# Kernel optimization log

Hardware: AMD Instinct MI355X
Metric: run time of the kernel (lower is better)

Reference implementation:

```python
import jax, jax.numpy as jnp
import numpy as np

B, T, E, H, L = 32, 2048, 256, 256, 2


def setup_inputs() -> dict:
    key = jax.random.key(0)
    k = jax.random.split(key, 6)
    x = jax.random.normal(k[0], (B, T, E), jnp.float32)
    h0 = jax.random.normal(k[1], (L, B, H), jnp.float32)
    # weights scaled to avoid tanh saturation (mimics fan-in init)
    W0 = jax.random.normal(k[2], (E + H, H), jnp.float32) * 0.05
    b0 = jax.random.normal(k[3], (H,), jnp.float32) * 0.05
    W1 = jax.random.normal(k[4], (2 * H, H), jnp.float32) * 0.05
    b1 = jax.random.normal(k[5], (H,), jnp.float32) * 0.05
    return {"x": x, "h0": h0, "W0": W0, "b0": b0, "W1": W1, "b1": b1}


def reference(x, h0, W0, b0, W1, b1):
    # x: [B,T,E]; h0: [L,B,H] (torch permutes to [B,L,H])
    h_init = jnp.transpose(h0, (1, 0, 2))  # [B,L,H]
    Ws = (W0, W1)
    bs = (b0, b1)

    def step(h, x_t):  # h: [B,L,H], x_t: [B,E]
        inp = x_t
        new_h = []
        for l in range(L):  # small fixed stack of cells
            z = jnp.concatenate([inp, h[:, l, :]], axis=-1) @ Ws[l] + bs[l]
            ht = jnp.tanh(z)  # [B,H]
            inp = ht
            new_h.append(ht)
        return jnp.stack(new_h, axis=1), ht  # carry, per-step top-layer output

    x_tbe = jnp.transpose(x, (1, 0, 2))  # [T,B,E]
    h_final, outs = jax.lax.scan(step, h_init, x_tbe)
    hidden_states = jnp.transpose(outs, (1, 0, 2))  # [B,T,H]
    ht = h_final[:, -1:, :]  # final top-layer state, [B,1,H]
    return hidden_states, ht
```

## Files before the change

### kernel.cpp

```cpp
#include <hip/hip_runtime.h>


typedef _Float16 half2_t __attribute__((ext_vector_type(2)));

#define TT 2048
#define BB 32
#define XPB 8
#define CHUNK 64
#define NCHUNK (TT / CHUNK)

__device__ __forceinline__ unsigned packw(float lo, float hi) {
    half2_t r;
    r.x = (_Float16)lo;
    r.y = (_Float16)hi;
    return __builtin_bit_cast(unsigned, r);
}
#define H2(X) __builtin_bit_cast(half2_t, (X))

#define LDS_BARRIER() asm volatile("s_waitcnt lgkmcnt(0)\n\ts_barrier" ::: "memory")

__device__ __forceinline__ int rload(int* pf) {
    return __hip_atomic_load(pf, __ATOMIC_RELAXED, __HIP_MEMORY_SCOPE_AGENT);
}
__device__ __forceinline__ void astore(int* pf, int v) {
    __hip_atomic_store(pf, v, __ATOMIC_RELEASE, __HIP_MEMORY_SCOPE_AGENT);
}
#define ACQUIRE_FENCE() __builtin_amdgcn_fence(__ATOMIC_ACQUIRE, "agent")

#define KAW8(B)                                                             \
    "+v"(wp[(B)]), "+v"(wp[(B) + 1]), "+v"(wp[(B) + 2]), "+v"(wp[(B) + 3]), \
    "+v"(wp[(B) + 4]), "+v"(wp[(B) + 5]), "+v"(wp[(B) + 6]), "+v"(wp[(B) + 7])
#define KEEPALIVE()                                                  \
    asm volatile("" : KAW8(0), KAW8(8), KAW8(16), KAW8(24));         \
    asm volatile("" : KAW8(32), KAW8(40), KAW8(48), KAW8(56));       \
    asm volatile("" : KAW8(64), KAW8(72), KAW8(80), KAW8(88));       \
    asm volatile("" : KAW8(96), KAW8(104), KAW8(112), KAW8(120));

#define FDOT(H, W_, A) A = __builtin_amdgcn_fdot2(H2(H), H2(W_), A, false)
#define FD4(H, K)               \
    FDOT(H, wp[(K)], ac0);      \
    FDOT(H, wp[32 + (K)], ac1); \
    FDOT(H, wp[64 + (K)], ac2); \
    FDOT(H, wp[96 + (K)], ac3);

#define DOTS()                                                          \
    float ac0 = 0.f, ac1 = 0.f, ac2 = 0.f, ac3 = 0.f;                   \
    {                                                                   \
        const uint4* hp_ = hbq + 9 * p;                                 \
        uint4 q0 = hp_[0], q1 = hp_[1], q2 = hp_[2], q3 = hp_[3];       \
        uint4 q4 = hp_[4], q5 = hp_[5], q6 = hp_[6], q7 = hp_[7];       \
        FD4(q0.x, 0)  FD4(q0.y, 1)  FD4(q0.z, 2)  FD4(q0.w, 3)         \
        FD4(q1.x, 4)  FD4(q1.y, 5)  FD4(q1.z, 6)  FD4(q1.w, 7)         \
        FD4(q2.x, 8)  FD4(q2.y, 9)  FD4(q2.z, 10) FD4(q2.w, 11)        \
        FD4(q3.x, 12) FD4(q3.y, 13) FD4(q3.z, 14) FD4(q3.w, 15)        \
        FD4(q4.x, 16) FD4(q4.y, 17) FD4(q4.z, 18) FD4(q4.w, 19)        \
        FD4(q5.x, 20) FD4(q5.y, 21) FD4(q5.z, 22) FD4(q5.w, 23)        \
        FD4(q6.x, 24) FD4(q6.y, 25) FD4(q6.z, 26) FD4(q6.w, 27)        \
        FD4(q7.x, 28) FD4(q7.y, 29) FD4(q7.z, 30) FD4(q7.w, 31)        \
    }

#define BFLY(x)                                                              \
    asm("v_add_f32_dpp %0, %0, %0 quad_perm:[1,0,3,2] row_mask:0xf "         \
        "bank_mask:0xf"                                                      \
        : "+v"(x));                                                          \
    asm("v_add_f32_dpp %0, %0, %0 quad_perm:[2,3,0,1] row_mask:0xf "         \
        "bank_mask:0xf"                                                      \
        : "+v"(x));

#define LOAD_WP4(Wm, rowbase, p_, jg_)                                       \
    _Pragma("unroll")                                                        \
    for (int c = 0; c < 4; ++c) {                                            \
        _Pragma("unroll")                                                    \
        for (int k = 0; k < 32; ++k) {                                       \
            const int col_ = (jg_) + 64 * c;                                 \
            wp[c * 32 + k] =                                                 \
                packw((Wm)[(size_t)((rowbase) + 64 * (p_) + 2 * k) * 256 +   \
                           col_],                                            \
                      (Wm)[(size_t)((rowbase) + 64 * (p_) + 2 * k + 1) * 256 \
                           + col_]);                                         \
        }                                                                    \
    }

__device__ __forceinline__ int sidx_of(int i) {
    return 72 * (i >> 6) + (i & 63);
}

template <bool ALIAS>
__device__ __forceinline__ void proj_rows(
    const float* __restrict__ src, float* __restrict__ dst,
    unsigned (&wp)[128], float bj, int nrows, uint4 (*hb)[36], int tid,
    int p, int jg, int col)
{
    _Float16* st0 = reinterpret_cast<_Float16*>(hb[0]);
    _Float16* st1 = reinterpret_cast<_Float16*>(hb[1]);
    const int si = sidx_of(tid);
    st0[si] = (_Float16)src[tid];
    __syncthreads();
    for (int r = 0; r < nrows; ++r) {
        KEEPALIVE()
        _Float16* stn = (r & 1) ? st0 : st1;
        if (r + 1 < nrows) stn[si] = (_Float16)src[(size_t)(r + 1) * 256 + tid];
        const uint4* hbq = hb[r & 1];
        DOTS()
        BFLY(ac0) BFLY(ac1) BFLY(ac2) BFLY(ac3)
        float z = (p == 0) ? ac0 : ((p == 1) ? ac1 : ((p == 2) ? ac2 : ac3));
        dst[(size_t)r * 256 + col] = z + bj;
        if (ALIAS) __syncthreads();
        else LDS_BARRIER();
    }
}

template <bool WAIT, bool PUB>
__device__ __forceinline__ void scan_core(
    const float* __restrict__ W, const float* __restrict__ h_init,
    const float* __restrict__ xsrc, float* __restrict__ hdst, float* hfinal,
    int* pubflag, int* waitflags, uint4 (*hb)[36], int tid)
{
    const int p = tid & 3;
    const int jg = tid >> 2;
    const int col = jg + 64 * p;

    unsigned wp[128];
    LOAD_WP4(W, 256, p, jg)

    _Float16* hw0 = reinterpret_cast<_Float16*>(hb[0]);
    _Float16* hw1 = reinterpret_cast<_Float16*>(hb[1]);
    hw0[sidx_of(tid)] = (_Float16)h_init[tid];
    const int wsi = 72 * p + jg;

    float xpc[XPB], xpn[XPB], hs[XPB];

    auto step = [&](int t, float xp) -> float {
        KEEPALIVE()
        const uint4* hbq = hb[t & 1];
        DOTS()
        BFLY(ac0) BFLY(ac1) BFLY(ac2) BFLY(ac3)
        float z = (p == 0) ? ac0 : ((p == 1) ? ac1 : ((p == 2) ? ac2 : ac3));
        z += xp;
        const float e = __expf(2.0f * z);
        const float hn = 1.0f - 2.0f / (e + 1.0f);
        _Float16* dstw = ((t + 1) & 1) ? hw1 : hw0;
        dstw[wsi] = (_Float16)hn;
        LDS_BARRIER();
        return hn;
    };

    __syncthreads();
    for (int chunk = 0; chunk < NCHUNK; ++chunk) {
        const int tbase = chunk * CHUNK;
        if (WAIT) {
            while (rload(&waitflags[chunk]) == 0) __builtin_amdgcn_s_sleep(1);
            ACQUIRE_FENCE();
        }
#pragma unroll
        for (int u = 0; u < XPB; ++u)
            xpc[u] = xsrc[(size_t)(tbase + u) * 256 + col];
        for (int g = 0; g < CHUNK / XPB; ++g) {
            const int t0 = tbase + g * XPB;
            if (g + 1 < CHUNK / XPB) {
#pragma unroll
                for (int u = 0; u < XPB; ++u)
                    xpn[u] = xsrc[(size_t)(t0 + XPB + u) * 256 + col];
            }
#pragma unroll
            for (int u = 0; u < XPB; ++u) hs[u] = step(t0 + u, xpc[u]);
#pragma unroll
            for (int u = 0; u < XPB; ++u)
                hdst[(size_t)(t0 + u) * 256 + col] = hs[u];
            if (t0 + XPB == TT && hfinal != nullptr) hfinal[col] = hs[XPB - 1];
            if (g + 1 < CHUNK / XPB) {
#pragma unroll
                for (int u = 0; u < XPB; ++u) xpc[u] = xpn[u];
            }
        }
        if (PUB) {
            __syncthreads();
            if (tid == 0) astore(pubflag, tbase + CHUNK);
        }
    }
}

template <bool ALIAS>
__global__ __launch_bounds__(256, 1) void proj23_kernel(
    const float* in, const float* __restrict__ W, const float* __restrict__ bias,
    float* out, int rows_per_wg)
{
    __shared__ uint4 hb[2][36];
    const int tid = threadIdx.x;
    const int p = tid & 3;
    const int jg = tid >> 2;
    const int col = jg + 64 * p;
    unsigned wp[128];
    LOAD_WP4(W, 0, p, jg)
    const float bj = bias[col];
    const size_t r0 = (size_t)blockIdx.x * rows_per_wg;
    proj_rows<ALIAS>(in + r0 * 256, out + r0 * 256, wp, bj, rows_per_wg, hb,
                     tid, p, jg, col);
}

__global__ __launch_bounds__(256, 1) void scan23_kernel(
    const float* __restrict__ W, const float* __restrict__ h_init,
    float* __restrict__ io, float* __restrict__ hfinal)
{
    __shared__ uint4 hb[2][36];
    const int b = blockIdx.x;
    scan_core<false, false>(W, h_init + b * 256, io + (size_t)b * TT * 256,
                            io + (size_t)b * TT * 256,
                            hfinal ? hfinal + b * 256 : nullptr, nullptr,
                            nullptr, hb, threadIdx.x);
}

__global__ __launch_bounds__(256, 1) void mega23_kernel(
    const float* __restrict__ x, const float* __restrict__ W0,
    const float* __restrict__ b0v, const float* __restrict__ W1,
    const float* __restrict__ b1v, const float* __restrict__ h0init,
    float* xpA, float* out, int* flags)
{
    __shared__ uint4 hb[2][36];
    const int tid = threadIdx.x;
    const int bid = blockIdx.x;
    int* flagL0 = flags;
    int* chunkdone = flags + BB * 16;
    int* xp0done = flags + BB * 16 + BB * NCHUNK;

    if (bid < BB) {
        const int b = bid;
        scan_core<true, true>(W0, h0init + b * 256, xpA + (size_t)b * TT * 256,
                              out + (size_t)b * TT * 256, nullptr,
                              &flagL0[b * 16], &xp0done[b * NCHUNK], hb, tid);
    } else if (bid < 3 * BB) {
        const int k = bid - BB;
        const int b = k >> 1;
        const int half = k & 1;
        const int p = tid & 3;
        const int jg = tid >> 2;
        const int col = jg + 64 * p;

        unsigned wp[128];
        LOAD_WP4(W1, 0, p, jg)
        const float bj = b1v[col];

        for (int chunk = half; chunk < NCHUNK; chunk += 2) {
            while (rload(&flagL0[b * 16]) < (chunk + 1) * CHUNK)
                __builtin_amdgcn_s_sleep(1);
            ACQUIRE_FENCE();
            const int tbase = chunk * CHUNK;
            const float* src = out + ((size_t)b * TT + tbase) * 256;
            float* dst = xpA + ((size_t)b * TT + tbase) * 256;
            proj_rows<false>(src, dst, wp, bj, CHUNK, hb, tid, p, jg, col);
            __syncthreads();
            if (tid == 0) astore(&chunkdone[b * NCHUNK + chunk], 1);
        }
    } else if (bid < 4 * BB) {
        const int b = bid - 3 * BB;
        scan_core<true, false>(W1, h0init + (size_t)(BB + b) * 256,
                               xpA + (size_t)b * TT * 256,
                               out + (size_t)b * TT * 256,
                               out + (size_t)BB * TT * 256 + b * 256, nullptr,
                               &chunkdone[b * NCHUNK], hb, tid);
    } else {
        const int k = bid - 4 * BB;
        const int b = k >> 1;
        const int half = k & 1;
        const int p = tid & 3;
        const int jg = tid >> 2;
        const int col = jg + 64 * p;

        unsigned wp[128];
        LOAD_WP4(W0, 0, p, jg)
        const float bj = b0v[col];

        for (int chunk = half; chunk < NCHUNK; chunk += 2) {
            const int tbase = chunk * CHUNK;
            const float* src = x + ((size_t)b * TT + tbase) * 256;
            float* dst = xpA + ((size_t)b * TT + tbase) * 256;
            proj_rows<false>(src, dst, wp, bj, CHUNK, hb, tid, p, jg, col);
            __syncthreads();
            if (tid == 0) astore(&xp0done[b * NCHUNK + chunk], 1);
        }
    }
}

extern "C" void kernel_launch(void* const* d_in, const int* in_sizes, int n_in,
                              void* d_out, int out_size, void* d_ws, size_t ws_size,
                              hipStream_t stream) {
    const float* x  = (const float*)d_in[0];
    const float* h0 = (const float*)d_in[1];
    const float* W0 = (const float*)d_in[2];
    const float* b0 = (const float*)d_in[3];
    const float* W1 = (const float*)d_in[4];
    const float* b1 = (const float*)d_in[5];
    float* out = (float*)d_out;

    const size_t XPA_FLOATS = (size_t)BB * TT * 256;
    const size_t FLAG_INTS = (size_t)BB * 16 + 2 * (size_t)BB * NCHUNK;
    const size_t NEEDED = XPA_FLOATS * 4 + FLAG_INTS * 4;

    if (ws_size >= NEEDED) {
        float* xpA = (float*)d_ws;
        int* flags = (int*)((char*)d_ws + XPA_FLOATS * 4);
        hipMemsetAsync(flags, 0, FLAG_INTS * 4, stream);
        mega23_kernel<<<6 * BB, 256, 0, stream>>>(x, W0, b0, W1, b1, h0, xpA,
                                                  out, flags);
    } else {
        proj23_kernel<true><<<512, 256, 0, stream>>>(x, W0, b0, out, 128);
        scan23_kernel<<<BB, 256, 0, stream>>>(W0, h0, out, nullptr);
        proj23_kernel<true><<<512, 256, 0, stream>>>(out, W1, b1, out, 128);
        scan23_kernel<<<BB, 256, 0, stream>>>(W1, h0 + BB * 256, out,
                                              out + XPA_FLOATS);
    }
}
```

Baseline: 1.188 ms.

## Fuse layer-0 scan, layer-1 projection and layer-1 scan into one wavefront-pipelined workgroup

Replaces the multi-block mega kernel with two launches. A chaser kernel computes the layer-0 input projection into a workspace and sets per-chunk flags. A fused kernel then runs one 768-thread workgroup per batch element, where three 256-thread groups skew layer-0 recurrence, layer-1 input projection and layer-1 recurrence by one step each and exchange data through LDS ring buffers. This removes the global-memory round trip and cross-workgroup flag polling between layers, but every step now pays a 768-thread barrier and register pressure rises at the larger block size. XPB is also reduced from 8 to 4.

```diff
diff --git a/kernel.cpp b/kernel.cpp
--- a/kernel.cpp
+++ b/kernel.cpp
@@ -5,7 +5,7 @@
 
 #define TT 2048
 #define BB 32
-#define XPB 8
+#define XPB 4
 #define CHUNK 64
 #define NCHUNK (TT / CHUNK)
 
@@ -110,78 +110,179 @@
     }
 }
 
-template <bool WAIT, bool PUB>
-__device__ __forceinline__ void scan_core(
+__device__ __forceinline__ void scan_serial(
     const float* __restrict__ W, const float* __restrict__ h_init,
     const float* __restrict__ xsrc, float* __restrict__ hdst, float* hfinal,
-    int* pubflag, int* waitflags, uint4 (*hb)[36], int tid)
+    uint4 (*hb)[36], int tid)
 {
     const int p = tid & 3;
     const int jg = tid >> 2;
     const int col = jg + 64 * p;
-
     unsigned wp[128];
     LOAD_WP4(W, 256, p, jg)
-
     _Float16* hw0 = reinterpret_cast<_Float16*>(hb[0]);
     _Float16* hw1 = reinterpret_cast<_Float16*>(hb[1]);
     hw0[sidx_of(tid)] = (_Float16)h_init[tid];
     const int wsi = 72 * p + jg;
-
-    float xpc[XPB], xpn[XPB], hs[XPB];
-
-    auto step = [&](int t, float xp) -> float {
+    __syncthreads();
+    float hn = 0.f;
+    for (int t = 0; t < TT; ++t) {
         KEEPALIVE()
         const uint4* hbq = hb[t & 1];
         DOTS()
         BFLY(ac0) BFLY(ac1) BFLY(ac2) BFLY(ac3)
         float z = (p == 0) ? ac0 : ((p == 1) ? ac1 : ((p == 2) ? ac2 : ac3));
-        z += xp;
+        z += xsrc[(size_t)t * 256 + col];
         const float e = __expf(2.0f * z);
-        const float hn = 1.0f - 2.0f / (e + 1.0f);
+        hn = 1.0f - 2.0f / (e + 1.0f);
         _Float16* dstw = ((t + 1) & 1) ? hw1 : hw0;
         dstw[wsi] = (_Float16)hn;
+        hdst[(size_t)t * 256 + col] = hn;
         LDS_BARRIER();
-        return hn;
+    }
+    if (hfinal != nullptr) hfinal[col] = hn;
+}
+
+__global__ __launch_bounds__(256, 1) void chaser0_kernel(
+    const float* __restrict__ x, const float* __restrict__ W0,
+    const float* __restrict__ b0v, float* xpA, int* xp0done)
+{
+    __shared__ uint4 hb[2][36];
+    const int tid = threadIdx.x;
+    const int k = blockIdx.x;
+    const int b = k >> 2;
+    const int quarter = k & 3;
+    const int p = tid & 3;
+    const int jg = tid >> 2;
+    const int col = jg + 64 * p;
+
+    unsigned wp[128];
+    LOAD_WP4(W0, 0, p, jg)
+    const float bj = b0v[col];
+
+    for (int chunk = quarter; chunk < NCHUNK; chunk += 4) {
+        const int tbase = chunk * CHUNK;
+        const float* src = x + ((size_t)b * TT + tbase) * 256;
+        float* dst = xpA + ((size_t)b * TT + tbase) * 256;
+        proj_rows<false>(src, dst, wp, bj, CHUNK, hb, tid, p, jg, col);
+        __syncthreads();
+        if (tid == 0) astore(&xp0done[b * NCHUNK + chunk], 1);
+    }
+}
+
+__global__ __launch_bounds__(768, 3) void fused24_kernel(
+    const float* __restrict__ xpA, const float* __restrict__ W0,
+    const float* __restrict__ W1, const float* __restrict__ b1v,
+    const float* __restrict__ h0init, float* __restrict__ out, int* xp0done)
+{
+    __shared__ __align__(16) _Float16 h0ring[3][288];
+    __shared__ float xp1ring[2][264];
+    __shared__ __align__(16) _Float16 h1buf[2][288];
+
+    const int tid = threadIdx.x;
+    const int grp = tid >> 8;
+    const int ltid = tid & 255;
+    const int p = ltid & 3;
+    const int jg = ltid >> 2;
+    const int col = jg + 64 * p;
+    const int b = blockIdx.x;
+
+    unsigned wp[128];
+    if (grp == 0) {
+        LOAD_WP4(W0, 256, p, jg)
+    } else if (grp == 1) {
+        LOAD_WP4(W1, 0, p, jg)
+    } else {
+        LOAD_WP4(W1, 256, p, jg)
+    }
+    const float bj = (grp == 1) ? b1v[col] : 0.f;
+
+    if (grp == 0) h0ring[2][sidx_of(ltid)] = (_Float16)h0init[b * 256 + ltid];
+    if (grp == 2)
+        h1buf[0][sidx_of(ltid)] = (_Float16)h0init[(size_t)(BB + b) * 256 + ltid];
+
+    const float* xsrc = xpA + (size_t)b * TT * 256;
+    float* hdst = out + (size_t)b * TT * 256;
+    int* myflags = xp0done + b * NCHUNK;
+    __syncthreads();
+
+    float xpc[XPB], xpn[XPB];
+
+    auto STEP = [&](int s, float xp0) {
+        KEEPALIVE()
+        if (grp == 0) {
+            if (s < TT) {
+                const uint4* hbq = (const uint4*)h0ring[(s + 2) % 3];
+                DOTS()
+                BFLY(ac0) BFLY(ac1) BFLY(ac2) BFLY(ac3)
+                float z = (p == 0) ? ac0
+                        : (p == 1) ? ac1 : ((p == 2) ? ac2 : ac3);
+                z += xp0;
+                const float e = __expf(2.0f * z);
+                const float hn = 1.0f - 2.0f / (e + 1.0f);
+                h0ring[s % 3][72 * p + jg] = (_Float16)hn;
+            }
+        } else if (grp == 1) {
+            if (s >= 1 && s <= TT) {
+                const int t = s - 1;
+                const uint4* hbq = (const uint4*)h0ring[t % 3];
+                DOTS()
+                BFLY(ac0) BFLY(ac1) BFLY(ac2) BFLY(ac3)
+                float z = (p == 0) ? ac0
+                        : (p == 1) ? ac1 : ((p == 2) ? ac2 : ac3);
+                xp1ring[t & 1][66 * p + jg] = z + bj;
+            }
+        } else {
+            if (s >= 2) {
+                const int t = s - 2;
+                const float xp = xp1ring[t & 1][66 * p + jg];
+                const uint4* hbq = (const uint4*)h1buf[t & 1];
+                DOTS()
+                BFLY(ac0) BFLY(ac1) BFLY(ac2) BFLY(ac3)
+                float z = (p == 0) ? ac0
+                        : (p == 1) ? ac1 : ((p == 2) ? ac2 : ac3);
+                z += xp;
+                const float e = __expf(2.0f * z);
+                const float hn = 1.0f - 2.0f / (e + 1.0f);
+                h1buf[(t + 1) & 1][72 * p + jg] = (_Float16)hn;
+                hdst[(size_t)t * 256 + col] = hn;
+                if (t == TT - 1)
+                    out[(size_t)BB * TT * 256 + b * 256 + col] = hn;
+            }
+        }
+        LDS_BARRIER();
     };
 
-    __syncthreads();
     for (int chunk = 0; chunk < NCHUNK; ++chunk) {
         const int tbase = chunk * CHUNK;
-        if (WAIT) {
-            while (rload(&waitflags[chunk]) == 0) __builtin_amdgcn_s_sleep(1);
+        if (grp == 0) {
+            while (rload(&myflags[chunk]) == 0) __builtin_amdgcn_s_sleep(1);
             ACQUIRE_FENCE();
+#pragma unroll
+            for (int u = 0; u < XPB; ++u)
+                xpc[u] = xsrc[(size_t)(tbase + u) * 256 + col];
         }
-#pragma unroll
-        for (int u = 0; u < XPB; ++u)
-            xpc[u] = xsrc[(size_t)(tbase + u) * 256 + col];
         for (int g = 0; g < CHUNK / XPB; ++g) {
-            const int t0 = tbase + g * XPB;
-            if (g + 1 < CHUNK / XPB) {
+            const int s0 = tbase + g * XPB;
+            if (grp == 0 && g + 1 < CHUNK / XPB) {
 #pragma unroll
                 for (int u = 0; u < XPB; ++u)
-                    xpn[u] = xsrc[(size_t)(t0 + XPB + u) * 256 + col];
+                    xpn[u] = xsrc[(size_t)(s0 + XPB + u) * 256 + col];
             }
 #pragma unroll
-            for (int u = 0; u < XPB; ++u) hs[u] = step(t0 + u, xpc[u]);
-#pragma unroll
-            for (int u = 0; u < XPB; ++u)
-                hdst[(size_t)(t0 + u) * 256 + col] = hs[u];
-            if (t0 + XPB == TT && hfinal != nullptr) hfinal[col] = hs[XPB - 1];
-            if (g + 1 < CHUNK / XPB) {
+            for (int u = 0; u < XPB; ++u) STEP(s0 + u, xpc[u]);
+            if (grp == 0 && g + 1 < CHUNK / XPB) {
 #pragma unroll
                 for (int u = 0; u < XPB; ++u) xpc[u] = xpn[u];
             }
         }
-        if (PUB) {
-            __syncthreads();
-            if (tid == 0) astore(pubflag, tbase + CHUNK);
-        }
-    }
+    }
+    STEP(TT, 0.f);
+    STEP(TT + 1, 0.f);
 }
 
 template <bool ALIAS>
-__global__ __launch_bounds__(256, 1) void proj23_kernel(
+__global__ __launch_bounds__(256, 1) void proj24_kernel(
     const float* in, const float* __restrict__ W, const float* __restrict__ bias,
     float* out, int rows_per_wg)
 {
@@ -198,87 +299,15 @@
                      tid, p, jg, col);
 }
 
-__global__ __launch_bounds__(256, 1) void scan23_kernel(
+__global__ __launch_bounds__(256, 1) void scan24_kernel(
     const float* __restrict__ W, const float* __restrict__ h_init,
     float* __restrict__ io, float* __restrict__ hfinal)
 {
     __shared__ uint4 hb[2][36];
     const int b = blockIdx.x;
-    scan_core<false, false>(W, h_init + b * 256, io + (size_t)b * TT * 256,
-                            io + (size_t)b * TT * 256,
-                            hfinal ? hfinal + b * 256 : nullptr, nullptr,
-                            nullptr, hb, threadIdx.x);
-}
-
-__global__ __launch_bounds__(256, 1) void mega23_kernel(
-    const float* __restrict__ x, const float* __restrict__ W0,
-    const float* __restrict__ b0v, const float* __restrict__ W1,
-    const float* __restrict__ b1v, const float* __restrict__ h0init,
-    float* xpA, float* out, int* flags)
-{
-    __shared__ uint4 hb[2][36];
-    const int tid = threadIdx.x;
-    const int bid = blockIdx.x;
-    int* flagL0 = flags;
-    int* chunkdone = flags + BB * 16;
-    int* xp0done = flags + BB * 16 + BB * NCHUNK;
-
-    if (bid < BB) {
-        const int b = bid;
-        scan_core<true, true>(W0, h0init + b * 256, xpA + (size_t)b * TT * 256,
-                              out + (size_t)b * TT * 256, nullptr,
-                              &flagL0[b * 16], &xp0done[b * NCHUNK], hb, tid);
-    } else if (bid < 3 * BB) {
-        const int k = bid - BB;
-        const int b = k >> 1;
-        const int half = k & 1;
-        const int p = tid & 3;
-        const int jg = tid >> 2;
-        const int col = jg + 64 * p;
-
-        unsigned wp[128];
-        LOAD_WP4(W1, 0, p, jg)
-        const float bj = b1v[col];
-
-        for (int chunk = half; chunk < NCHUNK; chunk += 2) {
-            while (rload(&flagL0[b * 16]) < (chunk + 1) * CHUNK)
-                __builtin_amdgcn_s_sleep(1);
-            ACQUIRE_FENCE();
-            const int tbase = chunk * CHUNK;
-            const float* src = out + ((size_t)b * TT + tbase) * 256;
-            float* dst = xpA + ((size_t)b * TT + tbase) * 256;
-            proj_rows<false>(src, dst, wp, bj, CHUNK, hb, tid, p, jg, col);
-            __syncthreads();
-            if (tid == 0) astore(&chunkdone[b * NCHUNK + chunk], 1);
-        }
-    } else if (bid < 4 * BB) {
-        const int b = bid - 3 * BB;
-        scan_core<true, false>(W1, h0init + (size_t)(BB + b) * 256,
-                               xpA + (size_t)b * TT * 256,
-                               out + (size_t)b * TT * 256,
-                               out + (size_t)BB * TT * 256 + b * 256, nullptr,
-                               &chunkdone[b * NCHUNK], hb, tid);
-    } else {
-        const int k = bid - 4 * BB;
-        const int b = k >> 1;
-        const int half = k & 1;
-        const int p = tid & 3;
-        const int jg = tid >> 2;
-        const int col = jg + 64 * p;
-
-        unsigned wp[128];
-        LOAD_WP4(W0, 0, p, jg)
-        const float bj = b0v[col];
-
-        for (int chunk = half; chunk < NCHUNK; chunk += 2) {
-            const int tbase = chunk * CHUNK;
-            const float* src = x + ((size_t)b * TT + tbase) * 256;
-            float* dst = xpA + ((size_t)b * TT + tbase) * 256;
-            proj_rows<false>(src, dst, wp, bj, CHUNK, hb, tid, p, jg, col);
-            __syncthreads();
-            if (tid == 0) astore(&xp0done[b * NCHUNK + chunk], 1);
-        }
-    }
+    scan_serial(W, h_init + b * 256, io + (size_t)b * TT * 256,
+                io + (size_t)b * TT * 256,
+                hfinal ? hfinal + b * 256 : nullptr, hb, threadIdx.x);
 }
 
 extern "C" void kernel_launch(void* const* d_in, const int* in_sizes, int n_in,
@@ -293,20 +322,20 @@
     float* out = (float*)d_out;
 
     const size_t XPA_FLOATS = (size_t)BB * TT * 256;
-    const size_t FLAG_INTS = (size_t)BB * 16 + 2 * (size_t)BB * NCHUNK;
+    const size_t FLAG_INTS = (size_t)BB * NCHUNK;
     const size_t NEEDED = XPA_FLOATS * 4 + FLAG_INTS * 4;
 
     if (ws_size >= NEEDED) {
         float* xpA = (float*)d_ws;
         int* flags = (int*)((char*)d_ws + XPA_FLOATS * 4);
         hipMemsetAsync(flags, 0, FLAG_INTS * 4, stream);
-        mega23_kernel<<<6 * BB, 256, 0, stream>>>(x, W0, b0, W1, b1, h0, xpA,
-                                                  out, flags);
+        chaser0_kernel<<<4 * BB, 256, 0, stream>>>(x, W0, b0, xpA, flags);
+        fused24_kernel<<<BB, 768, 0, stream>>>(xpA, W0, W1, b1, h0, out, flags);
     } else {
-        proj23_kernel<true><<<512, 256, 0, stream>>>(x, W0, b0, out, 128);
-        scan23_kernel<<<BB, 256, 0, stream>>>(W0, h0, out, nullptr);
-        proj23_kernel<true><<<512, 256, 0, stream>>>(out, W1, b1, out, 128);
-        scan23_kernel<<<BB, 256, 0, stream>>>(W1, h0 + BB * 256, out,
+        proj24_kernel<true><<<512, 256, 0, stream>>>(x, W0, b0, out, 128);
+        scan24_kernel<<<BB, 256, 0, stream>>>(W0, h0, out, nullptr);
+        proj24_kernel<true><<<512, 256, 0, stream>>>(out, W1, b1, out, 128);
+        scan24_kernel<<<BB, 256, 0, stream>>>(W1, h0 + BB * 256, out,
                                               out + XPA_FLOATS);
     }
 }
```

Result: slower. 3.184 ms (+168.0%).
